# Optimization experiments

Measured on AMD Instinct MI355X. Metric: run time of the kernel, lower is better.

## Reference

```python
import jax, jax.numpy as jnp
import numpy as np

B, DIN, DOUT = 8192, 1024, 1024


def setup_inputs() -> dict:
    key = jax.random.key(0)
    ks = jax.random.split(key, 20)
    s = 0.02  # weight init scale to keep gate pre-activations sane
    inp = {
        "x": jax.random.normal(ks[0], (B, DIN), jnp.float32),
        "h": jax.random.normal(ks[1], (B, DOUT), jnp.float32),
        "c": jax.random.normal(ks[2], (B, DOUT), jnp.float32),
    }
    names = ["i", "f", "g", "o"]
    k = 3
    for n in names:
        inp[f"Wx{n}"] = jax.random.normal(ks[k], (DIN, DOUT), jnp.float32) * s; k += 1
        inp[f"Wh{n}"] = jax.random.normal(ks[k], (DOUT, DOUT), jnp.float32) * s; k += 1
        inp[f"bx{n}"] = jax.random.normal(ks[k], (DOUT,), jnp.float32) * s; k += 1
        inp[f"bh{n}"] = jax.random.normal(ks[k], (DOUT,), jnp.float32) * s; k += 1
    return inp


def reference(x, h, c,
              Wxi, Whi, bxi, bhi,
              Wxf, Whf, bxf, bhf,
              Wxg, Whg, bxg, bhg,
              Wxo, Who, bxo, bho):
    # Fuse the 8 separate Linear layers into 2 GEMMs on concatenated weights
    # (same math as summing per-gate x/h projections + both biases).
    Wx = jnp.concatenate([Wxi, Wxf, Wxg, Wxo], axis=1)   # [DIN, 4*DOUT]
    Wh = jnp.concatenate([Whi, Whf, Whg, Who], axis=1)   # [DOUT, 4*DOUT]
    b = jnp.concatenate([bxi + bhi, bxf + bhf, bxg + bhg, bxo + bho])  # [4*DOUT]
    z = x @ Wx + h @ Wh + b                               # [B, 4*DOUT]
    zi, zf, zg, zo = jnp.split(z, 4, axis=1)
    i = jax.nn.sigmoid(zi)
    f = jax.nn.sigmoid(zf)
    g = jnp.tanh(zg)
    o = jax.nn.sigmoid(zo)
    c_new = f * c + i * g
    h_new = o * jnp.tanh(c_new)
    return (h_new, c_new)
```

## Files before the change

### kernel.cpp

```cpp
#include <hip/hip_runtime.h>
#include <stdint.h>


typedef __attribute__((ext_vector_type(4))) int i32x4;
typedef __attribute__((ext_vector_type(8))) _Float16 half8;
typedef __attribute__((ext_vector_type(4))) _Float16 half4;
typedef __attribute__((ext_vector_type(4))) float f32x4;

__device__ __forceinline__ void gload_lds16(const void* g, void* l) {
  __builtin_amdgcn_global_load_lds(
      (const __attribute__((address_space(1))) void*)g,
      (__attribute__((address_space(3))) void*)l, 16, 0, 0);
}

__device__ __forceinline__ float sigf(float x) { return 1.0f / (1.0f + __expf(-x)); }
__device__ __forceinline__ float tanhf_(float x) { return 1.0f - 2.0f / (__expf(2.0f * x) + 1.0f); }
__device__ __forceinline__ int q8(float v, float s) {
  int q = (int)rintf(v * s);
  return q < -127 ? -127 : (q > 127 ? 127 : q);
}

#define FENCE asm volatile("" ::: "memory")
#define BAR do { FENCE; __builtin_amdgcn_s_barrier(); FENCE; } while (0)
#define LG0 do { asm volatile("s_waitcnt lgkmcnt(0)" ::: "memory"); \
                 __builtin_amdgcn_sched_barrier(0); } while (0)
#define VMC(n) asm volatile("s_waitcnt vmcnt(" #n ")" ::: "memory")

__global__ void lstm_colmax(const float* __restrict__ Wxi, const float* __restrict__ Wxf,
                            const float* __restrict__ Wxg, const float* __restrict__ Wxo,
                            const float* __restrict__ Whi, const float* __restrict__ Whf,
                            const float* __restrict__ Whg, const float* __restrict__ Who,
                            unsigned int* __restrict__ colmax) {
  __shared__ float cm[1024];
  int b = blockIdx.x, t = threadIdx.x;
  int m = b >> 6;
  int r0 = (b & 63) * 16;
  const float* Ws[8] = {Wxi, Wxf, Wxg, Wxo, Whi, Whf, Whg, Who};
  const float* src = Ws[m] + (size_t)r0 * 1024;
  #pragma unroll
  for (int i = 0; i < 4; ++i) cm[t + 256 * i] = 0.f;
  __syncthreads();
  for (int r = 0; r < 16; ++r) {
    #pragma unroll
    for (int c4 = 0; c4 < 4; ++c4) {
      int col = t + 256 * c4;
      float v = fabsf(src[(size_t)r * 1024 + col]);
      cm[col] = fmaxf(cm[col], v);
    }
  }
  __syncthreads();
  int g = m & 3;
  #pragma unroll
  for (int i = 0; i < 4; ++i) {
    int j = t + 256 * i;
    int np = ((j >> 4) << 6) + g * 16 + (j & 15);
    atomicMax(&colmax[np], __float_as_uint(cm[j]));
  }
}

__global__ void lstm_quant(const float* __restrict__ x, const float* __restrict__ h,
                           const float* __restrict__ Wxi, const float* __restrict__ Whi,
                           const float* __restrict__ Wxf, const float* __restrict__ Whf,
                           const float* __restrict__ Wxg, const float* __restrict__ Whg,
                           const float* __restrict__ Wxo, const float* __restrict__ Who,
                           const float* __restrict__ bxi, const float* __restrict__ bhi,
                           const float* __restrict__ bxf, const float* __restrict__ bhf,
                           const float* __restrict__ bxg, const float* __restrict__ bhg,
                           const float* __restrict__ bxo, const float* __restrict__ bho,
                           const unsigned int* __restrict__ colmax,
                           signed char* __restrict__ Wt, signed char* __restrict__ Xh,
                           float* __restrict__ bias, float* __restrict__ sxd) {
  int b = blockIdx.x, t = threadIdx.x;
  if (b < 8192) {
    __shared__ float wm[4];
    int row = b;
    int k = t * 8;
    const float* src = (k < 1024) ? (x + (size_t)row * 1024 + k)
                                  : (h + (size_t)row * 1024 + (k - 1024));
    float4 f0 = *(const float4*)src;
    float4 f1 = *(const float4*)(src + 4);
    float v[8] = {f0.x, f0.y, f0.z, f0.w, f1.x, f1.y, f1.z, f1.w};
    float m = 0.f;
    #pragma unroll
    for (int e = 0; e < 8; ++e) m = fmaxf(m, fabsf(v[e]));
    #pragma unroll
    for (int off = 32; off; off >>= 1) m = fmaxf(m, __shfl_xor(m, off));
    if ((t & 63) == 0) wm[t >> 6] = m;
    __syncthreads();
    m = fmaxf(fmaxf(wm[0], wm[1]), fmaxf(wm[2], wm[3]));
    m = fmaxf(m, 1e-12f);
    float sq = 127.f / m;
    uint64_t w = 0;
    #pragma unroll
    for (int e = 0; e < 8; ++e) {
      int q = q8(v[e], sq);
      w |= ((uint64_t)(uint32_t)(q & 0xFF)) << (8 * e);
    }
    *(uint64_t*)(Xh + (size_t)row * 2048 + k) = w;
    if (t == 0) sxd[row] = m * (1.f / 127.f);
  } else if (b < 16384) {
    __shared__ float tile[32][33];
    int bb = b - 8192;
    int nt = bb & 127, kt = bb >> 7;
    int g = nt & 3, jt32 = nt >> 2;
    const float* Wx[4] = {Wxi, Wxf, Wxg, Wxo};
    const float* Wh[4] = {Whi, Whf, Whg, Who};
    int k0 = kt * 32;
    const float* src = (k0 < 1024) ? (Wx[g] + (size_t)k0 * 1024)
                                   : (Wh[g] + (size_t)(k0 - 1024) * 1024);
    int j0 = jt32 * 32;
    int cc = t & 31, r0 = t >> 5;
    #pragma unroll
    for (int p = 0; p < 4; ++p) {
      int r = p * 8 + r0;
      tile[r][cc] = src[(size_t)r * 1024 + j0 + cc];
    }
    __syncthreads();
    int jj = t >> 3, kk = (t & 7) * 4;
    int j = j0 + jj;
    int np = ((j >> 4) << 6) + g * 16 + (j & 15);
    float mw = fmaxf(__uint_as_float(colmax[np]), 1e-12f);
    float sq = 127.f / mw;
    uint32_t w = 0;
    #pragma unroll
    for (int e = 0; e < 4; ++e) {
      int q = q8(tile[kk + e][jj], sq);
      w |= ((uint32_t)(q & 0xFF)) << (8 * e);
    }
    *(uint32_t*)(Wt + (size_t)np * 2048 + k0 + kk) = w;
  } else {
    int tt = (b - 16384) * 256 + t;
    if (tt < 4096) {
      const float* bx[4] = {bxi, bxf, bxg, bxo};
      const float* bh[4] = {bhi, bhf, bhg, bho};
      int q = tt >> 4, r = tt & 15;
      int g = q & 3, j = (q >> 2) * 16 + r;
      bias[tt] = bx[g][j] + bh[g][j];
    }
  }
}

__global__ __launch_bounds__(512, 2) void lstm_gemm_i8(
    const signed char* __restrict__ Xh, const signed char* __restrict__ Wt,
    const float* __restrict__ c, const float* __restrict__ bias,
    const float* __restrict__ sxd, const unsigned int* __restrict__ colmax,
    float* __restrict__ out) {
  __shared__ signed char sA[2][256 * 64];
  __shared__ signed char sB[2][256 * 64];

  int bid = blockIdx.x;
  int xcd = bid & 7, idx = bid >> 3;
  int mt = (xcd >> 1) * 8 + (idx >> 3);
  int jt = (xcd & 1) * 8 + (idx & 7);
  int brow0 = mt * 256, bcol0 = jt * 256;

  int tid = threadIdx.x, lane = tid & 63, wave = tid >> 6;
  int wr = wave >> 2, wc = wave & 3;
  int l15 = lane & 15, l4 = lane >> 4;

  i32x4 acc[8][4] = {};

  int roff = (l4 ^ ((l15 >> 1) & 3)) * 16;
  int aoff0 = (wr * 128 + l15) * 64;
  int boff0 = (wc * 64 + l15) * 64;
  int ssl = ((tid & 3) ^ ((tid >> 3) & 3)) * 16;
  int srow = tid >> 2;

  auto stA = [&](int buf, int t, int a) {
    const signed char* src = Xh + (size_t)(brow0 + a * 128 + srow) * 2048 + t * 64 + ssl;
    gload_lds16(src, &sA[buf][(a * 128 + wave * 16) * 64]);
  };
  auto stB = [&](int buf, int t, int a) {
    const signed char* src = Wt + (size_t)(bcol0 + a * 128 + srow) * 2048 + t * 64 + ssl;
    gload_lds16(src, &sB[buf][(a * 128 + wave * 16) * 64]);
  };

#define STA(buf, t) do { stA(buf, t, 0); stA(buf, t, 1); } while (0)
#define STB(buf, t) do { stB(buf, t, 0); stB(buf, t, 1); } while (0)

#define LDBA(BUF) do { _Pragma("unroll") for (int nf = 0; nf < 4; ++nf) \
    bf[nf] = *(const i32x4*)&sB[BUF][boff0 + nf * 16 * 64 + roff]; } while (0)
#define LDAH(mh, BUF) do { _Pragma("unroll") for (int mi = 0; mi < 4; ++mi) \
    af[mi] = *(const i32x4*)&sA[BUF][aoff0 + ((mh) * 4 + mi) * 16 * 64 + roff]; } while (0)
#define MMH(mh) do {                                                          \
    __builtin_amdgcn_s_setprio(1);                                            \
    _Pragma("unroll") for (int mi = 0; mi < 4; ++mi)                          \
    _Pragma("unroll") for (int nf = 0; nf < 4; ++nf)                          \
      acc[(mh) * 4 + mi][nf] = __builtin_amdgcn_mfma_i32_16x16x64_i8(         \
          af[mi], bf[nf], acc[(mh) * 4 + mi][nf], 0, 0, 0);                   \
    __builtin_amdgcn_s_setprio(0); } while (0)

  STA(0, 0); STB(0, 0); STB(1, 1);
  VMC(2);
  BAR;

  i32x4 af[4], bf[4];

#pragma unroll 1
  for (int i = 0; i < 16; ++i) {
    const int u = 2 * i + 1, v = 2 * i + 2, w = 2 * i + 3;
    const bool pf = (i < 15);

    STA(1, u);
    LDBA(0); LDAH(0, 0);
    LG0; MMH(0);
    BAR;

    if (pf) STB(0, v);
    LDAH(1, 0);
    LG0; MMH(1);
    if (pf) { VMC(2); }
    else    { VMC(0); }
    BAR;

    if (pf) STA(0, v);
    LDBA(1); LDAH(0, 1);
    LG0; MMH(0);
    BAR;

    if (pf) STB(1, w);
    LDAH(1, 1);
    LG0; MMH(1);
    if (pf) { VMC(2); }
    BAR;
  }
#undef STA
#undef STB
#undef LDBA
#undef LDAH
#undef MMH

  int j = jt * 64 + wc * 16 + l15;
  int nbase = bcol0 + wc * 64 + l15;
  const float inv127 = 1.f / 127.f;
  float sw0 = fmaxf(__uint_as_float(colmax[nbase + 0]),  1e-12f) * inv127;
  float sw1 = fmaxf(__uint_as_float(colmax[nbase + 16]), 1e-12f) * inv127;
  float sw2 = fmaxf(__uint_as_float(colmax[nbase + 32]), 1e-12f) * inv127;
  float sw3 = fmaxf(__uint_as_float(colmax[nbase + 48]), 1e-12f) * inv127;
  float bi  = bias[nbase + 0];
  float bff = bias[nbase + 16];
  float bg  = bias[nbase + 32];
  float bo  = bias[nbase + 48];
  float* hout = out;
  float* cout = out + (size_t)8192 * 1024;
  #pragma unroll
  for (int m = 0; m < 8; ++m) {
    #pragma unroll
    for (int r = 0; r < 4; ++r) {
      int grow = brow0 + wr * 128 + m * 16 + l4 * 4 + r;
      float sx = sxd[grow];
      size_t o = (size_t)grow * 1024 + j;
      float zi = (float)acc[m][0][r] * (sx * sw0) + bi;
      float zf = (float)acc[m][1][r] * (sx * sw1) + bff;
      float zg = (float)acc[m][2][r] * (sx * sw2) + bg;
      float zo = (float)acc[m][3][r] * (sx * sw3) + bo;
      float ig = sigf(zi);
      float fg = sigf(zf);
      float gg = tanhf_(zg);
      float og = sigf(zo);
      float cold = c[o];
      float cn = fg * cold + ig * gg;
      hout[o] = og * tanhf_(cn);
      cout[o] = cn;
    }
  }
}


__global__ void lstm_pack_w_v1(const float* __restrict__ Wxi, const float* __restrict__ Whi,
                               const float* __restrict__ Wxf, const float* __restrict__ Whf,
                               const float* __restrict__ Wxg, const float* __restrict__ Whg,
                               const float* __restrict__ Wxo, const float* __restrict__ Who,
                               _Float16* __restrict__ Wt) {
  __shared__ float tile[32][33];
  int nt = blockIdx.x;
  int kt = blockIdx.y;
  int g = nt & 3, jt = nt >> 2;
  const float* Wx[4] = {Wxi, Wxf, Wxg, Wxo};
  const float* Wh[4] = {Whi, Whf, Whg, Who};
  int k0 = kt * 32;
  const float* src = (k0 < 1024) ? (Wx[g] + (size_t)k0 * 1024)
                                 : (Wh[g] + (size_t)(k0 - 1024) * 1024);
  int j0 = jt * 32;
  int t = threadIdx.x;
  int cc = t & 31, r0 = t >> 5;
  #pragma unroll
  for (int p = 0; p < 4; ++p) {
    int r = p * 8 + r0;
    tile[r][cc] = src[(size_t)r * 1024 + j0 + cc];
  }
  __syncthreads();
  int jj = t >> 3, kk = (t & 7) * 4;
  half4 v;
  v[0] = (_Float16)tile[kk + 0][jj];
  v[1] = (_Float16)tile[kk + 1][jj];
  v[2] = (_Float16)tile[kk + 2][jj];
  v[3] = (_Float16)tile[kk + 3][jj];
  _Float16* dst = Wt + (size_t)(nt * 32 + jj) * 2048 + k0 + kk;
  *(half4*)dst = v;
}

__global__ void lstm_pack_bias_v1(const float* __restrict__ bxi, const float* __restrict__ bhi,
                                  const float* __restrict__ bxf, const float* __restrict__ bhf,
                                  const float* __restrict__ bxg, const float* __restrict__ bhg,
                                  const float* __restrict__ bxo, const float* __restrict__ bho,
                                  float* __restrict__ bias) {
  int t = blockIdx.x * 256 + threadIdx.x;
  if (t >= 4096) return;
  const float* bx[4] = {bxi, bxf, bxg, bxo};
  const float* bh[4] = {bhi, bhf, bhg, bho};
  int jt = t >> 7, g = (t >> 5) & 3, jj = t & 31;
  int j = jt * 32 + jj;
  bias[t] = bx[g][j] + bh[g][j];
}

__global__ __launch_bounds__(256, 2) void lstm_gemm_v1(
    const float* __restrict__ x, const float* __restrict__ h, const float* __restrict__ c,
    const _Float16* __restrict__ Wt, const float* __restrict__ bias,
    float* __restrict__ out) {
  __shared__ ushort sA[128 * 64];
  __shared__ ushort sB[128 * 64];
  int bid = blockIdx.x;
  int sbid = (bid & 7) * 256 + (bid >> 3);
  int mt = sbid >> 5, jt = sbid & 31;
  int brow0 = mt * 128;
  int tid = threadIdx.x;
  int lane = tid & 63, wave = tid >> 6;
  int wr = wave >> 1, wc = wave & 1;
  f32x4 acc[4][4] = {};
  int ar = tid >> 3;
  int as = tid & 7;
  int l3 = lane >> 3, l7w = lane & 7;
  int bsw = ((l7w ^ l3) << 3);
  int l15 = lane & 15, l4 = lane >> 4, l7 = lane & 7;
  for (int kt = 0; kt < 32; ++kt) {
    int k0 = kt * 64;
    const float* asrc = (k0 < 1024) ? (x + k0) : (h + (k0 - 1024));
    #pragma unroll
    for (int stp = 0; stp < 4; ++stp) {
      int row = stp * 32 + ar;
      const float* p = asrc + (size_t)(brow0 + row) * 1024 + as * 8;
      float4 f0 = *(const float4*)p;
      float4 f1 = *(const float4*)(p + 4);
      half8 hv;
      hv[0] = (_Float16)f0.x; hv[1] = (_Float16)f0.y;
      hv[2] = (_Float16)f0.z; hv[3] = (_Float16)f0.w;
      hv[4] = (_Float16)f1.x; hv[5] = (_Float16)f1.y;
      hv[6] = (_Float16)f1.z; hv[7] = (_Float16)f1.w;
      *(half8*)&sA[row * 64 + ((as ^ (row & 7)) << 3)] = hv;
    }
    #pragma unroll
    for (int ccall = 0; ccall < 4; ++ccall) {
      int rowbase = ccall * 32 + wave * 8;
      int grow = jt * 128 + rowbase + l3;
      const _Float16* src = Wt + (size_t)grow * 2048 + k0 + bsw;
      gload_lds16(src, &sB[rowbase * 64]);
    }
    __syncthreads();
    #pragma unroll
    for (int ks = 0; ks < 2; ++ks) {
      half8 af[4], bfr[4];
      #pragma unroll
      for (int mi = 0; mi < 4; ++mi) {
        int row = wr * 64 + mi * 16 + l15;
        af[mi] = *(const half8*)&sA[row * 64 + (((ks * 4 + l4) ^ l7) << 3)];
      }
      #pragma unroll
      for (int g = 0; g < 4; ++g) {
        int nr = g * 32 + wc * 16 + l15;
        bfr[g] = *(const half8*)&sB[nr * 64 + (((ks * 4 + l4) ^ l7) << 3)];
      }
      #pragma unroll
      for (int mi = 0; mi < 4; ++mi)
        #pragma unroll
        for (int g = 0; g < 4; ++g)
          acc[mi][g] = __builtin_amdgcn_mfma_f32_16x16x32_f16(af[mi], bfr[g], acc[mi][g], 0, 0, 0);
    }
    __syncthreads();
  }
  int j = jt * 32 + wc * 16 + l15;
  int nb = jt * 128 + wc * 16 + l15;
  float bi  = bias[nb + 0];
  float bff = bias[nb + 32];
  float bg  = bias[nb + 64];
  float bo  = bias[nb + 96];
  float* hout = out;
  float* cout = out + (size_t)8192 * 1024;
  #pragma unroll
  for (int mi = 0; mi < 4; ++mi) {
    #pragma unroll
    for (int r = 0; r < 4; ++r) {
      int grow = brow0 + wr * 64 + mi * 16 + l4 * 4 + r;
      size_t idx = (size_t)grow * 1024 + j;
      float zi = acc[mi][0][r] + bi;
      float zf = acc[mi][1][r] + bff;
      float zg = acc[mi][2][r] + bg;
      float zo = acc[mi][3][r] + bo;
      float ig = sigf(zi);
      float fg = sigf(zf);
      float gg = tanhf_(zg);
      float og = sigf(zo);
      float cold = c[idx];
      float cn = fg * cold + ig * gg;
      hout[idx] = og * tanhf_(cn);
      cout[idx] = cn;
    }
  }
}

extern "C" void kernel_launch(void* const* d_in, const int* in_sizes, int n_in,
                              void* d_out, int out_size, void* d_ws, size_t ws_size,
                              hipStream_t stream) {
  const float* x   = (const float*)d_in[0];
  const float* h   = (const float*)d_in[1];
  const float* c   = (const float*)d_in[2];
  const float* Wxi = (const float*)d_in[3];
  const float* Whi = (const float*)d_in[4];
  const float* bxi = (const float*)d_in[5];
  const float* bhi = (const float*)d_in[6];
  const float* Wxf = (const float*)d_in[7];
  const float* Whf = (const float*)d_in[8];
  const float* bxf = (const float*)d_in[9];
  const float* bhf = (const float*)d_in[10];
  const float* Wxg = (const float*)d_in[11];
  const float* Whg = (const float*)d_in[12];
  const float* bxg = (const float*)d_in[13];
  const float* bhg = (const float*)d_in[14];
  const float* Wxo = (const float*)d_in[15];
  const float* Who = (const float*)d_in[16];
  const float* bxo = (const float*)d_in[17];
  const float* bho = (const float*)d_in[18];
  float* out = (float*)d_out;

  const size_t WT_B = (size_t)4096 * 2048;
  const size_t XH_B = (size_t)8192 * 2048;
  const size_t NEED = WT_B + XH_B + 4096 * 4 + 8192 * 4 + 4096 * 4;

  if (ws_size >= NEED) {
    signed char* Wt = (signed char*)d_ws;
    signed char* Xh = (signed char*)d_ws + WT_B;
    char* p = (char*)d_ws + WT_B + XH_B;
    float* bias = (float*)p;               p += 4096 * 4;
    float* sxd  = (float*)p;               p += 8192 * 4;
    unsigned int* colmax = (unsigned int*)p;
    hipMemsetAsync(colmax, 0, 4096 * 4, stream);
    lstm_colmax<<<512, 256, 0, stream>>>(Wxi, Wxf, Wxg, Wxo, Whi, Whf, Whg, Who, colmax);
    lstm_quant<<<16400, 256, 0, stream>>>(x, h, Wxi, Whi, Wxf, Whf, Wxg, Whg,
                                          Wxo, Who, bxi, bhi, bxf, bhf,
                                          bxg, bhg, bxo, bho, colmax,
                                          Wt, Xh, bias, sxd);
    lstm_gemm_i8<<<512, 512, 0, stream>>>(Xh, Wt, c, bias, sxd, colmax, out);
  } else {
    _Float16* Wt = (_Float16*)d_ws;
    float* bias  = (float*)((char*)d_ws + (size_t)4096 * 2048 * 2);
    lstm_pack_w_v1<<<dim3(128, 64), 256, 0, stream>>>(Wxi, Whi, Wxf, Whf, Wxg, Whg, Wxo, Who, Wt);
    lstm_pack_bias_v1<<<16, 256, 0, stream>>>(bxi, bhi, bxf, bhf, bxg, bhg, bxo, bho, bias);
    lstm_gemm_v1<<<2048, 256, 0, stream>>>(x, h, c, Wt, bias, out);
  }
}
```

Before: 135.6 us.

## Switch int8 GEMM mainloop to triple-buffered LDS with one barrier per k-step

Replaces the double-buffered, four-half-step schedule of the int8 MFMA GEMM with a three-stage LDS ring. Each k-step prefetches the tile two steps ahead, loads all A and B fragments, runs all 32 MFMAs, then waits and synchronises once. The aim is to cut barriers and give the global-to-LDS loads more time to hide behind compute. The cost is 96KB of LDS per block instead of 64KB and eight live A fragments per wave. That likely stops two 512-thread blocks from sharing a CU and raises register pressure.

```diff
diff --git a/kernel.cpp b/kernel.cpp
--- a/kernel.cpp
+++ b/kernel.cpp
@@ -140,13 +140,13 @@
   }
 }
 
-__global__ __launch_bounds__(512, 2) void lstm_gemm_i8(
+__global__ __launch_bounds__(512, 2) void lstm_gemm_i8r(
     const signed char* __restrict__ Xh, const signed char* __restrict__ Wt,
     const float* __restrict__ c, const float* __restrict__ bias,
     const float* __restrict__ sxd, const unsigned int* __restrict__ colmax,
     float* __restrict__ out) {
-  __shared__ signed char sA[2][256 * 64];
-  __shared__ signed char sB[2][256 * 64];
+  __shared__ signed char sA[3][256 * 64];
+  __shared__ signed char sB[3][256 * 64];
 
   int bid = blockIdx.x;
   int xcd = bid & 7, idx = bid >> 3;
@@ -175,60 +175,44 @@
     gload_lds16(src, &sB[buf][(a * 128 + wave * 16) * 64]);
   };
 
-#define STA(buf, t) do { stA(buf, t, 0); stA(buf, t, 1); } while (0)
-#define STB(buf, t) do { stB(buf, t, 0); stB(buf, t, 1); } while (0)
-
-#define LDBA(BUF) do { _Pragma("unroll") for (int nf = 0; nf < 4; ++nf) \
-    bf[nf] = *(const i32x4*)&sB[BUF][boff0 + nf * 16 * 64 + roff]; } while (0)
-#define LDAH(mh, BUF) do { _Pragma("unroll") for (int mi = 0; mi < 4; ++mi) \
-    af[mi] = *(const i32x4*)&sA[BUF][aoff0 + ((mh) * 4 + mi) * 16 * 64 + roff]; } while (0)
-#define MMH(mh) do {                                                          \
+#define STAGE(buf, t) do { stA(buf, t, 0); stA(buf, t, 1); \
+                           stB(buf, t, 0); stB(buf, t, 1); } while (0)
+
+#define LD_ALL(BUF) do {                                                      \
+    _Pragma("unroll") for (int nf = 0; nf < 4; ++nf)                          \
+      bf[nf] = *(const i32x4*)&sB[BUF][boff0 + nf * 16 * 64 + roff];          \
+    _Pragma("unroll") for (int mi = 0; mi < 8; ++mi)                          \
+      af[mi] = *(const i32x4*)&sA[BUF][aoff0 + mi * 16 * 64 + roff]; } while (0)
+#define MM_ALL() do {                                                         \
     __builtin_amdgcn_s_setprio(1);                                            \
-    _Pragma("unroll") for (int mi = 0; mi < 4; ++mi)                          \
+    _Pragma("unroll") for (int mi = 0; mi < 8; ++mi)                          \
     _Pragma("unroll") for (int nf = 0; nf < 4; ++nf)                          \
-      acc[(mh) * 4 + mi][nf] = __builtin_amdgcn_mfma_i32_16x16x64_i8(         \
-          af[mi], bf[nf], acc[(mh) * 4 + mi][nf], 0, 0, 0);                   \
+      acc[mi][nf] = __builtin_amdgcn_mfma_i32_16x16x64_i8(                    \
+          af[mi], bf[nf], acc[mi][nf], 0, 0, 0);                              \
     __builtin_amdgcn_s_setprio(0); } while (0)
 
-  STA(0, 0); STB(0, 0); STB(1, 1);
-  VMC(2);
+  STAGE(0, 0); STAGE(1, 1);
+  VMC(4);
   BAR;
 
-  i32x4 af[4], bf[4];
-
+  i32x4 af[8], bf[4];
+
+  int rb = 0, wb = 2;
 #pragma unroll 1
-  for (int i = 0; i < 16; ++i) {
-    const int u = 2 * i + 1, v = 2 * i + 2, w = 2 * i + 3;
-    const bool pf = (i < 15);
-
-    STA(1, u);
-    LDBA(0); LDAH(0, 0);
-    LG0; MMH(0);
+  for (int t = 0; t < 32; ++t) {
+    if (t < 30) STAGE(wb, t + 2);
+    LD_ALL(rb);
+    MM_ALL();
+    LG0;
+    if (t < 30)      { VMC(4); }
+    else if (t == 30){ VMC(0); }
     BAR;
-
-    if (pf) STB(0, v);
-    LDAH(1, 0);
-    LG0; MMH(1);
-    if (pf) { VMC(2); }
-    else    { VMC(0); }
-    BAR;
-
-    if (pf) STA(0, v);
-    LDBA(1); LDAH(0, 1);
-    LG0; MMH(0);
-    BAR;
-
-    if (pf) STB(1, w);
-    LDAH(1, 1);
-    LG0; MMH(1);
-    if (pf) { VMC(2); }
-    BAR;
-  }
-#undef STA
-#undef STB
-#undef LDBA
-#undef LDAH
-#undef MMH
+    rb = (rb == 2) ? 0 : rb + 1;
+    wb = (wb == 2) ? 0 : wb + 1;
+  }
+#undef STAGE
+#undef LD_ALL
+#undef MM_ALL
 
   int j = jt * 64 + wc * 16 + l15;
   int nbase = bcol0 + wc * 64 + l15;
@@ -449,7 +433,7 @@
                                           Wxo, Who, bxi, bhi, bxf, bhf,
                                           bxg, bhg, bxo, bho, colmax,
                                           Wt, Xh, bias, sxd);
-    lstm_gemm_i8<<<512, 512, 0, stream>>>(Xh, Wt, c, bias, sxd, colmax, out);
+    lstm_gemm_i8r<<<512, 512, 0, stream>>>(Xh, Wt, c, bias, sxd, colmax, out);
   } else {
     _Float16* Wt = (_Float16*)d_ws;
     float* bias  = (float*)((char*)d_ws + (size_t)4096 * 2048 * 2);
```

Result: slower. 153.4 us (+13.1%).

## Switch int8 LSTM GEMM to 32x32x32 MFMA with 32-wide gate interleave

Applied to the files above, without the earlier changes.

Replaces the 16x16x64 int8 MFMA tiling with 32x32x32 int8 MFMAs. The wave layout changes from 2x4 to 4x2 and the weight column interleave grows from 16 to 32 per gate, so each wave's output tile still contains all four gates for the fused epilogue. The colmax, quantization and bias packing index maps are updated to match. The intent is fewer LDS fragment loads per MFMA and denser matrix-core issue. It risks a different LDS bank-conflict pattern and a larger accumulator register footprint in the epilogue.

```diff
diff --git a/kernel.cpp b/kernel.cpp
--- a/kernel.cpp
+++ b/kernel.cpp
@@ -3,6 +3,7 @@
 
 
 typedef __attribute__((ext_vector_type(4))) int i32x4;
+typedef __attribute__((ext_vector_type(16))) int i32x16;
 typedef __attribute__((ext_vector_type(8))) _Float16 half8;
 typedef __attribute__((ext_vector_type(4))) _Float16 half4;
 typedef __attribute__((ext_vector_type(4))) float f32x4;
@@ -53,7 +54,7 @@
   #pragma unroll
   for (int i = 0; i < 4; ++i) {
     int j = t + 256 * i;
-    int np = ((j >> 4) << 6) + g * 16 + (j & 15);
+    int np = ((j >> 5) << 7) + g * 32 + (j & 31);
     atomicMax(&colmax[np], __float_as_uint(cm[j]));
   }
 }
@@ -117,8 +118,7 @@
     }
     __syncthreads();
     int jj = t >> 3, kk = (t & 7) * 4;
-    int j = j0 + jj;
-    int np = ((j >> 4) << 6) + g * 16 + (j & 15);
+    int np = jt32 * 128 + g * 32 + jj;
     float mw = fmaxf(__uint_as_float(colmax[np]), 1e-12f);
     float sq = 127.f / mw;
     uint32_t w = 0;
@@ -133,14 +133,15 @@
     if (tt < 4096) {
       const float* bx[4] = {bxi, bxf, bxg, bxo};
       const float* bh[4] = {bhi, bhf, bhg, bho};
-      int q = tt >> 4, r = tt & 15;
-      int g = q & 3, j = (q >> 2) * 16 + r;
+      int blk = tt >> 7, rem = tt & 127;
+      int g = rem >> 5, jl = rem & 31;
+      int j = blk * 32 + jl;
       bias[tt] = bx[g][j] + bh[g][j];
     }
   }
 }
 
-__global__ __launch_bounds__(512, 2) void lstm_gemm_i8(
+__global__ __launch_bounds__(512, 2) void lstm_gemm_i8w(
     const signed char* __restrict__ Xh, const signed char* __restrict__ Wt,
     const float* __restrict__ c, const float* __restrict__ bias,
     const float* __restrict__ sxd, const unsigned int* __restrict__ colmax,
@@ -155,14 +156,14 @@
   int brow0 = mt * 256, bcol0 = jt * 256;
 
   int tid = threadIdx.x, lane = tid & 63, wave = tid >> 6;
-  int wr = wave >> 2, wc = wave & 3;
-  int l15 = lane & 15, l4 = lane >> 4;
-
-  i32x4 acc[8][4] = {};
-
-  int roff = (l4 ^ ((l15 >> 1) & 3)) * 16;
-  int aoff0 = (wr * 128 + l15) * 64;
-  int boff0 = (wc * 64 + l15) * 64;
+  int mw = wave >> 1, wn = wave & 1;
+  int l31 = lane & 31, l5 = lane >> 5;
+
+  i32x16 acc[2][4] = {};
+
+  int f3 = (l31 >> 1) & 3;
+  int roff0 = ((0 + l5) ^ f3) * 16;
+  int roff1 = ((2 + l5) ^ f3) * 16;
   int ssl = ((tid & 3) ^ ((tid >> 3) & 3)) * 16;
   int srow = tid >> 2;
 
@@ -178,23 +179,28 @@
 #define STA(buf, t) do { stA(buf, t, 0); stA(buf, t, 1); } while (0)
 #define STB(buf, t) do { stB(buf, t, 0); stB(buf, t, 1); } while (0)
 
-#define LDBA(BUF) do { _Pragma("unroll") for (int nf = 0; nf < 4; ++nf) \
-    bf[nf] = *(const i32x4*)&sB[BUF][boff0 + nf * 16 * 64 + roff]; } while (0)
-#define LDAH(mh, BUF) do { _Pragma("unroll") for (int mi = 0; mi < 4; ++mi) \
-    af[mi] = *(const i32x4*)&sA[BUF][aoff0 + ((mh) * 4 + mi) * 16 * 64 + roff]; } while (0)
-#define MMH(mh) do {                                                          \
-    __builtin_amdgcn_s_setprio(1);                                            \
-    _Pragma("unroll") for (int mi = 0; mi < 4; ++mi)                          \
-    _Pragma("unroll") for (int nf = 0; nf < 4; ++nf)                          \
-      acc[(mh) * 4 + mi][nf] = __builtin_amdgcn_mfma_i32_16x16x64_i8(         \
-          af[mi], bf[nf], acc[(mh) * 4 + mi][nf], 0, 0, 0);                   \
+#define LDBA(BUF) do { _Pragma("unroll") for (int g2 = 0; g2 < 4; ++g2) { \
+    const signed char* p_ = &sB[BUF][(wn * 128 + g2 * 32 + l31) * 64];     \
+    bf[g2][0] = *(const i32x4*)(p_ + roff0);                               \
+    bf[g2][1] = *(const i32x4*)(p_ + roff1); } } while (0)
+#define LDAH(mh, BUF) do {                                                  \
+    const signed char* p_ = &sA[BUF][(mw * 64 + (mh) * 32 + l31) * 64];     \
+    af[0] = *(const i32x4*)(p_ + roff0);                                    \
+    af[1] = *(const i32x4*)(p_ + roff1); } while (0)
+#define MMH(mh) do {                                                        \
+    __builtin_amdgcn_s_setprio(1);                                          \
+    _Pragma("unroll") for (int g2 = 0; g2 < 4; ++g2) {                      \
+      i32x16 t_ = acc[mh][g2];                                              \
+      t_ = __builtin_amdgcn_mfma_i32_32x32x32_i8(af[0], bf[g2][0], t_, 0, 0, 0); \
+      t_ = __builtin_amdgcn_mfma_i32_32x32x32_i8(af[1], bf[g2][1], t_, 0, 0, 0); \
+      acc[mh][g2] = t_; }                                                   \
     __builtin_amdgcn_s_setprio(0); } while (0)
 
   STA(0, 0); STB(0, 0); STB(1, 1);
   VMC(2);
   BAR;
 
-  i32x4 af[4], bf[4];
+  i32x4 af[2], bf[4][2];
 
 #pragma unroll 1
   for (int i = 0; i < 16; ++i) {
@@ -230,30 +236,30 @@
 #undef LDAH
 #undef MMH
 
-  int j = jt * 64 + wc * 16 + l15;
-  int nbase = bcol0 + wc * 64 + l15;
+  int j = jt * 64 + wn * 32 + l31;
+  int nb = bcol0 + wn * 128 + l31;
   const float inv127 = 1.f / 127.f;
-  float sw0 = fmaxf(__uint_as_float(colmax[nbase + 0]),  1e-12f) * inv127;
-  float sw1 = fmaxf(__uint_as_float(colmax[nbase + 16]), 1e-12f) * inv127;
-  float sw2 = fmaxf(__uint_as_float(colmax[nbase + 32]), 1e-12f) * inv127;
-  float sw3 = fmaxf(__uint_as_float(colmax[nbase + 48]), 1e-12f) * inv127;
-  float bi  = bias[nbase + 0];
-  float bff = bias[nbase + 16];
-  float bg  = bias[nbase + 32];
-  float bo  = bias[nbase + 48];
+  float sw0 = fmaxf(__uint_as_float(colmax[nb + 0]),  1e-12f) * inv127;
+  float sw1 = fmaxf(__uint_as_float(colmax[nb + 32]), 1e-12f) * inv127;
+  float sw2 = fmaxf(__uint_as_float(colmax[nb + 64]), 1e-12f) * inv127;
+  float sw3 = fmaxf(__uint_as_float(colmax[nb + 96]), 1e-12f) * inv127;
+  float bi  = bias[nb + 0];
+  float bff = bias[nb + 32];
+  float bg  = bias[nb + 64];
+  float bo  = bias[nb + 96];
   float* hout = out;
   float* cout = out + (size_t)8192 * 1024;
   #pragma unroll
-  for (int m = 0; m < 8; ++m) {
-    #pragma unroll
-    for (int r = 0; r < 4; ++r) {
-      int grow = brow0 + wr * 128 + m * 16 + l4 * 4 + r;
+  for (int mi = 0; mi < 2; ++mi) {
+    #pragma unroll
+    for (int r = 0; r < 16; ++r) {
+      int grow = brow0 + mw * 64 + mi * 32 + (r & 3) + 8 * (r >> 2) + 4 * l5;
       float sx = sxd[grow];
       size_t o = (size_t)grow * 1024 + j;
-      float zi = (float)acc[m][0][r] * (sx * sw0) + bi;
-      float zf = (float)acc[m][1][r] * (sx * sw1) + bff;
-      float zg = (float)acc[m][2][r] * (sx * sw2) + bg;
-      float zo = (float)acc[m][3][r] * (sx * sw3) + bo;
+      float zi = (float)acc[mi][0][r] * (sx * sw0) + bi;
+      float zf = (float)acc[mi][1][r] * (sx * sw1) + bff;
+      float zg = (float)acc[mi][2][r] * (sx * sw2) + bg;
+      float zo = (float)acc[mi][3][r] * (sx * sw3) + bo;
       float ig = sigf(zi);
       float fg = sigf(zf);
       float gg = tanhf_(zg);
@@ -449,7 +455,7 @@
                                           Wxo, Who, bxi, bhi, bxf, bhf,
                                           bxg, bhg, bxo, bho, colmax,
                                           Wt, Xh, bias, sxd);
-    lstm_gemm_i8<<<512, 512, 0, stream>>>(Xh, Wt, c, bias, sxd, colmax, out);
+    lstm_gemm_i8w<<<512, 512, 0, stream>>>(Xh, Wt, c, bias, sxd, colmax, out);
   } else {
     _Float16* Wt = (_Float16*)d_ws;
     float* bias  = (float*)((char*)d_ws + (size_t)4096 * 2048 * 2);
```

After: 146.1 us. 1.08x slower.
